# Kernel tuning notes

Hardware: AMD Instinct MI355X
Metric: run time of the kernel (lower is better)

## Reference

```python
import jax, jax.numpy as jnp
import numpy as np


def setup_inputs() -> dict:
    key = jax.random.key(0)
    k1, k2, k3, k4 = jax.random.split(key, 4)
    B, L, H, E = 2, 10000, 8, 64
    NE = 160000
    return {
        "queries": jax.random.normal(k1, (B, L, H, E), dtype=jnp.float32),
        "keys": jax.random.normal(k2, (B, L, H, E), dtype=jnp.float32),
        "values": jax.random.normal(k3, (B, L, H, E), dtype=jnp.float32),
        "adj": jax.random.randint(k4, (2, NE), 0, L, dtype=jnp.int64),
    }


def reference(queries, keys, values, adj):
    # queries/keys/values: [B, L, H, E]; adj: [2, NE] (row 0 = dst group, row 1 = src)
    B, L, H, E = queries.shape
    softmax_temp = 1.0 / (E ** 0.5)
    dst = adj[0]
    src = adj[1]

    # edge-gather dot product: qk[b, e, h] = sum_d q[b, dst[e], h, d] * k[b, src[e], h, d]
    qk = jnp.sum(queries[:, dst] * keys[:, src], axis=-1) * softmax_temp  # [B, NE, H]

    # segment softmax grouped by destination node (dropout is identity at eval)
    qk_e = qk.transpose(1, 0, 2)  # [NE, B, H] (segment ops act on leading axis)
    seg_max = jax.ops.segment_max(qk_e, dst, num_segments=L)  # [L, B, H]
    ex = jnp.exp(qk_e - seg_max[dst])
    seg_sum = jax.ops.segment_sum(ex, dst, num_segments=L)  # [L, B, H]
    alpha = ex / (seg_sum[dst] + 1e-16)  # [NE, B, H]

    # spmm: gather v at src, weight by alpha, scatter-add to dst
    weighted = values[:, src] * alpha.transpose(1, 0, 2)[..., None]  # [B, NE, H, E]
    out = jnp.zeros_like(values).at[:, dst].add(weighted)  # [B, L, H, E]
    return out
```

## Files before the change

### kernel.cpp

```cpp
#include <hip/hip_runtime.h>

#define BB 2
#define HH 8
#define EE 64
#define ROW (HH * EE)
#define HC 4

typedef float vf4 __attribute__((ext_vector_type(4)));

__device__ inline unsigned short f2bf(float f) {
  unsigned int u = __float_as_uint(f);
  u = (u + 0x7fffu + ((u >> 16) & 1u)) >> 16;
  return (unsigned short)u;
}

__global__ __launch_bounds__(256) void convert_hist_kernel(
    const float* __restrict__ k, const float* __restrict__ v,
    unsigned short* __restrict__ kbf, unsigned short* __restrict__ vbf,
    const int* __restrict__ dst, int* __restrict__ counts,
    int n4, int NE) {
  int i = blockIdx.x * blockDim.x + threadIdx.x;
  if (i < n4) {
    vf4 kf = __builtin_nontemporal_load((const vf4*)k + i);
    vf4 vf = __builtin_nontemporal_load((const vf4*)v + i);
    ((ushort4*)kbf)[i] = make_ushort4(f2bf(kf.x), f2bf(kf.y), f2bf(kf.z), f2bf(kf.w));
    ((ushort4*)vbf)[i] = make_ushort4(f2bf(vf.x), f2bf(vf.y), f2bf(vf.z), f2bf(vf.w));
  }
  if (i < NE) {
    atomicAdd(&counts[dst[i]], 1);
  }
}

__global__ __launch_bounds__(1024) void scan_kernel(
    const int* __restrict__ counts_in, int* __restrict__ counts_mut,
    int* __restrict__ offsets, int L) {
  __shared__ int sums[1024];
  int tid = threadIdx.x;
  int chunk = (L + 1023) / 1024;
  int beg = tid * chunk;
  int end = min(beg + chunk, L);
  int s = 0;
  for (int i = beg; i < end; ++i) s += counts_in[i];
  sums[tid] = s;
  __syncthreads();
  for (int off = 1; off < 1024; off <<= 1) {
    int val = 0;
    if (tid >= off) val = sums[tid - off];
    __syncthreads();
    if (tid >= off) sums[tid] += val;
    __syncthreads();
  }
  int run = (tid > 0) ? sums[tid - 1] : 0;
  for (int i = beg; i < end; ++i) {
    offsets[i] = run;
    run += counts_in[i];
    counts_mut[i] = 0;
  }
  if (tid == 1023) offsets[L] = run;
}

__global__ __launch_bounds__(256) void fill_csr_kernel(
    const int* __restrict__ dst, const int* __restrict__ src,
    const int* __restrict__ offsets, int* __restrict__ cursor,
    int* __restrict__ csr_src, int NE) {
  int e = blockIdx.x * blockDim.x + threadIdx.x;
  if (e >= NE) return;
  int d = dst[e];
  int pos = atomicAdd(&cursor[d], 1);
  csr_src[offsets[d] + pos] = src[e];
}

__device__ inline void bf8_unpack(uint4 u, float* f) {
  f[0] = __uint_as_float(u.x << 16);
  f[1] = __uint_as_float(u.x & 0xffff0000u);
  f[2] = __uint_as_float(u.y << 16);
  f[3] = __uint_as_float(u.y & 0xffff0000u);
  f[4] = __uint_as_float(u.z << 16);
  f[5] = __uint_as_float(u.z & 0xffff0000u);
  f[6] = __uint_as_float(u.w << 16);
  f[7] = __uint_as_float(u.w & 0xffff0000u);
}

#define LOAD_HC(KK, VV, TT)                                           \
  _Pragma("unroll") for (int i_ = 0; i_ < HC; ++i_) {                 \
    int e_ = min((TT) + i_, NEm1);                                    \
    unsigned s_ = (unsigned)csr_src[e_];                              \
    KK[i_] = kb_base[s_ * (unsigned)(ROW / 8) + lane];                \
    VV[i_] = vb_base[s_ * (unsigned)(ROW / 8) + lane];                \
  }

#define COMPUTE_HC(KK, VV, TT)                                        \
  do {                                                                \
    float qk_[HC];                                                    \
    float cmax_ = -INFINITY;                                          \
    _Pragma("unroll") for (int i_ = 0; i_ < HC; ++i_) {               \
      float kf_[8];                                                   \
      bf8_unpack(KK[i_], kf_);                                        \
      float p_ = q0.x * kf_[0] + q0.y * kf_[1] + q0.z * kf_[2] +      \
                 q0.w * kf_[3] + q1.x * kf_[4] + q1.y * kf_[5] +      \
                 q1.z * kf_[6] + q1.w * kf_[7];                       \
      p_ += __shfl_xor(p_, 1);                                        \
      p_ += __shfl_xor(p_, 2);                                        \
      p_ += __shfl_xor(p_, 4);                                        \
      p_ = ((TT) + i_ < end) ? p_ : -INFINITY;                        \
      qk_[i_] = p_;                                                   \
      cmax_ = fmaxf(cmax_, p_);                                       \
    }                                                                 \
    if (__any(cmax_ > m)) {        \
      float mnew_ = fmaxf(m, cmax_);                                  \
      float scale_ = __expf(m - mnew_); \
      l_run *= scale_;                                                \
      _Pragma("unroll") for (int j_ = 0; j_ < 8; ++j_) acc[j_] *= scale_; \
      m = mnew_;                                                      \
    }                                                                 \
    _Pragma("unroll") for (int i_ = 0; i_ < HC; ++i_) {               \
      float a_ = __expf(qk_[i_] - m);        \
      l_run += a_;                                                    \
      float vfv_[8];                                                  \
      bf8_unpack(VV[i_], vfv_);                                       \
      _Pragma("unroll") for (int j_ = 0; j_ < 8; ++j_)                \
          acc[j_] += a_ * vfv_[j_];                                   \
    }                                                                 \
  } while (0)

__global__ __launch_bounds__(256, 4) void fused_attn_kernel(
    const float* __restrict__ q, const unsigned short* __restrict__ kbf,
    const unsigned short* __restrict__ vbf, const int* __restrict__ offsets,
    const int* __restrict__ csr_src, float* __restrict__ out, int L, int NE) {
  int wid = blockIdx.x * (blockDim.x >> 6) + (threadIdx.x >> 6);
  int lane = threadIdx.x & 63;
  if (wid >= L * BB) return;
  int d = wid >> 1;
  int b = wid & 1;
  int beg = offsets[d];
  int end = offsets[d + 1];
  const int NEm1 = NE - 1;

  const vf4* qrow = (const vf4*)(q + ((size_t)b * L + d) * ROW);
  vf4 q0 = __builtin_nontemporal_load(qrow + lane * 2 + 0);
  vf4 q1 = __builtin_nontemporal_load(qrow + lane * 2 + 1);
  q0 *= 0.125f;
  q1 *= 0.125f;

  float m = -INFINITY;
  float l_run = 0.0f;
  float acc[8];
#pragma unroll
  for (int i = 0; i < 8; ++i) acc[i] = 0.0f;

  const uint4* kb_base = (const uint4*)(kbf + (size_t)b * L * ROW);
  const uint4* vb_base = (const uint4*)(vbf + (size_t)b * L * ROW);

  uint4 kA[HC], vA[HC], kB[HC], vB[HC];
  int tA = beg;
  int tB = beg + HC;
  if (tA < end) {
    LOAD_HC(kA, vA, tA);
    LOAD_HC(kB, vB, tB);
    for (;;) {
      COMPUTE_HC(kA, vA, tA);
      tA = tB + HC;
      if (tA < end) LOAD_HC(kA, vA, tA);
      if (tB >= end) break;
      COMPUTE_HC(kB, vB, tB);
      tB = tA + HC;
      if (tB < end) LOAD_HC(kB, vB, tB);
      if (tA >= end) break;
    }
  }

  float r = 1.0f / (l_run + 1e-16f);
  vf4* orow = (vf4*)(out + ((size_t)b * L + d) * ROW);
  vf4 o0 = {acc[0] * r, acc[1] * r, acc[2] * r, acc[3] * r};
  vf4 o1 = {acc[4] * r, acc[5] * r, acc[6] * r, acc[7] * r};
  __builtin_nontemporal_store(o0, orow + lane * 2 + 0);
  __builtin_nontemporal_store(o1, orow + lane * 2 + 1);
}

extern "C" void kernel_launch(void* const* d_in, const int* in_sizes, int n_in,
                              void* d_out, int out_size, void* d_ws, size_t ws_size,
                              hipStream_t stream) {
  const float* q = (const float*)d_in[0];
  const float* k = (const float*)d_in[1];
  const float* v = (const float*)d_in[2];
  const int* adj = (const int*)d_in[3];

  const int NE = in_sizes[3] / 2;
  const int L = in_sizes[0] / (BB * HH * EE);
  const int* dst = adj;
  const int* src = adj + NE;
  const int nelem = BB * L * HH * EE;

  char* ws = (char*)d_ws;
  size_t off = 0;
  unsigned short* kbf = (unsigned short*)(ws + off); off += (size_t)nelem * 2;
  unsigned short* vbf = (unsigned short*)(ws + off); off += (size_t)nelem * 2;
  int* counts = (int*)(ws + off);   off += (size_t)L * 4;
  int* offsets = (int*)(ws + off);  off += (size_t)(L + 1) * 4;
  int* csr_src = (int*)(ws + off);  off += (size_t)NE * 4;

  hipMemsetAsync(counts, 0, (size_t)L * 4, stream);

  int n4 = nelem / 4;
  convert_hist_kernel<<<(n4 + 255) / 256, 256, 0, stream>>>(
      k, v, kbf, vbf, dst, counts, n4, NE);

  scan_kernel<<<1, 1024, 0, stream>>>(counts, counts, offsets, L);

  fill_csr_kernel<<<(NE + 255) / 256, 256, 0, stream>>>(
      dst, src, offsets, counts, csr_src, NE);

  int nwaves = L * BB;
  fused_attn_kernel<<<(nwaves + 3) / 4, 256, 0, stream>>>(
      q, kbf, vbf, offsets, csr_src, (float*)d_out, L, NE);
}
```

Baseline: 306.9 us.

## Use grid-stride persistent waves and batched 8-edge loads in fused attention

```diff
diff --git a/kernel.cpp b/kernel.cpp
--- a/kernel.cpp
+++ b/kernel.cpp
@@ -81,100 +81,92 @@
   f[7] = __uint_as_float(u.w & 0xffff0000u);
 }
 
-#define LOAD_HC(KK, VV, TT)                                           \
-  _Pragma("unroll") for (int i_ = 0; i_ < HC; ++i_) {                 \
-    int e_ = min((TT) + i_, NEm1);                                    \
-    unsigned s_ = (unsigned)csr_src[e_];                              \
-    KK[i_] = kb_base[s_ * (unsigned)(ROW / 8) + lane];                \
-    VV[i_] = vb_base[s_ * (unsigned)(ROW / 8) + lane];                \
-  }
-
-#define COMPUTE_HC(KK, VV, TT)                                        \
-  do {                                                                \
-    float qk_[HC];                                                    \
-    float cmax_ = -INFINITY;                                          \
-    _Pragma("unroll") for (int i_ = 0; i_ < HC; ++i_) {               \
-      float kf_[8];                                                   \
-      bf8_unpack(KK[i_], kf_);                                        \
-      float p_ = q0.x * kf_[0] + q0.y * kf_[1] + q0.z * kf_[2] +      \
-                 q0.w * kf_[3] + q1.x * kf_[4] + q1.y * kf_[5] +      \
-                 q1.z * kf_[6] + q1.w * kf_[7];                       \
-      p_ += __shfl_xor(p_, 1);                                        \
-      p_ += __shfl_xor(p_, 2);                                        \
-      p_ += __shfl_xor(p_, 4);                                        \
-      p_ = ((TT) + i_ < end) ? p_ : -INFINITY;                        \
-      qk_[i_] = p_;                                                   \
-      cmax_ = fmaxf(cmax_, p_);                                       \
-    }                                                                 \
-    if (__any(cmax_ > m)) {        \
-      float mnew_ = fmaxf(m, cmax_);                                  \
-      float scale_ = __expf(m - mnew_); \
-      l_run *= scale_;                                                \
-      _Pragma("unroll") for (int j_ = 0; j_ < 8; ++j_) acc[j_] *= scale_; \
-      m = mnew_;                                                      \
-    }                                                                 \
-    _Pragma("unroll") for (int i_ = 0; i_ < HC; ++i_) {               \
-      float a_ = __expf(qk_[i_] - m);        \
-      l_run += a_;                                                    \
-      float vfv_[8];                                                  \
-      bf8_unpack(VV[i_], vfv_);                                       \
-      _Pragma("unroll") for (int j_ = 0; j_ < 8; ++j_)                \
-          acc[j_] += a_ * vfv_[j_];                                   \
-    }                                                                 \
-  } while (0)
-
-__global__ __launch_bounds__(256, 4) void fused_attn_kernel(
+__global__ __launch_bounds__(256) void fused_attn_kernel(
     const float* __restrict__ q, const unsigned short* __restrict__ kbf,
     const unsigned short* __restrict__ vbf, const int* __restrict__ offsets,
-    const int* __restrict__ csr_src, float* __restrict__ out, int L, int NE) {
-  int wid = blockIdx.x * (blockDim.x >> 6) + (threadIdx.x >> 6);
-  int lane = threadIdx.x & 63;
-  if (wid >= L * BB) return;
-  int d = wid >> 1;
-  int b = wid & 1;
-  int beg = offsets[d];
-  int end = offsets[d + 1];
-  const int NEm1 = NE - 1;
-
-  const vf4* qrow = (const vf4*)(q + ((size_t)b * L + d) * ROW);
-  vf4 q0 = __builtin_nontemporal_load(qrow + lane * 2 + 0);
-  vf4 q1 = __builtin_nontemporal_load(qrow + lane * 2 + 1);
-  q0 *= 0.125f;
-  q1 *= 0.125f;
-
-  float m = -INFINITY;
-  float l_run = 0.0f;
-  float acc[8];
-#pragma unroll
-  for (int i = 0; i < 8; ++i) acc[i] = 0.0f;
-
-  const uint4* kb_base = (const uint4*)(kbf + (size_t)b * L * ROW);
-  const uint4* vb_base = (const uint4*)(vbf + (size_t)b * L * ROW);
-
-  uint4 kA[HC], vA[HC], kB[HC], vB[HC];
-  int tA = beg;
-  int tB = beg + HC;
-  if (tA < end) {
-    LOAD_HC(kA, vA, tA);
-    LOAD_HC(kB, vB, tB);
-    for (;;) {
-      COMPUTE_HC(kA, vA, tA);
-      tA = tB + HC;
-      if (tA < end) LOAD_HC(kA, vA, tA);
-      if (tB >= end) break;
-      COMPUTE_HC(kB, vB, tB);
-      tB = tA + HC;
-      if (tB < end) LOAD_HC(kB, vB, tB);
-      if (tA >= end) break;
+    const int* __restrict__ csr_src, float* __restrict__ out, int L) {
+  const int lane = threadIdx.x & 63;
+  const int wslot = blockIdx.x * (blockDim.x >> 6) + (threadIdx.x >> 6);
+  const int wstride = gridDim.x * (blockDim.x >> 6);
+  const int nwid = L * BB;
+
+  for (int wid = wslot; wid < nwid; wid += wstride) {
+    int d = wid >> 1;
+    int b = wid & 1;
+    int beg = offsets[d];
+    int end = offsets[d + 1];
+
+    const vf4* qrow = (const vf4*)(q + ((size_t)b * L + d) * ROW);
+    vf4 q0 = __builtin_nontemporal_load(qrow + lane * 2 + 0);
+    vf4 q1 = __builtin_nontemporal_load(qrow + lane * 2 + 1);
+    q0 *= 0.125f;
+    q1 *= 0.125f;
+
+    float m = -INFINITY;
+    float l_run = 0.0f;
+    float acc[8];
+#pragma unroll
+    for (int i = 0; i < 8; ++i) acc[i] = 0.0f;
+
+    const uint4* kb_base = (const uint4*)(kbf + (size_t)b * L * ROW);
+    const uint4* vb_base = (const uint4*)(vbf + (size_t)b * L * ROW);
+
+    for (int t0 = beg; t0 < end; t0 += 2 * HC) {
+      int cnt = min(2 * HC, end - t0);
+      uint4 kk[2 * HC], vv[2 * HC];
+#pragma unroll
+      for (int i = 0; i < 2 * HC; ++i) {
+        if (i < cnt) {
+          unsigned s = (unsigned)csr_src[t0 + i];
+          kk[i] = kb_base[s * (unsigned)(ROW / 8) + lane];
+          vv[i] = vb_base[s * (unsigned)(ROW / 8) + lane];
+        }
+      }
+      float qk[2 * HC];
+      float cmax = -INFINITY;
+#pragma unroll
+      for (int i = 0; i < 2 * HC; ++i) {
+        qk[i] = -INFINITY;
+        if (i < cnt) {
+          float kf[8];
+          bf8_unpack(kk[i], kf);
+          float p = q0.x * kf[0] + q0.y * kf[1] + q0.z * kf[2] + q0.w * kf[3] +
+                    q1.x * kf[4] + q1.y * kf[5] + q1.z * kf[6] + q1.w * kf[7];
+          p += __shfl_xor(p, 1);
+          p += __shfl_xor(p, 2);
+          p += __shfl_xor(p, 4);
+          qk[i] = p;
+          cmax = fmaxf(cmax, p);
+        }
+      }
+      if (__any(cmax > m)) {
+        float mnew = fmaxf(m, cmax);
+        float scale = __expf(m - mnew);
+        l_run *= scale;
+#pragma unroll
+        for (int i = 0; i < 8; ++i) acc[i] *= scale;
+        m = mnew;
+      }
+#pragma unroll
+      for (int i = 0; i < 2 * HC; ++i) {
+        if (i < cnt) {
+          float a = __expf(qk[i] - m);
+          l_run += a;
+          float vf[8];
+          bf8_unpack(vv[i], vf);
+#pragma unroll
+          for (int j = 0; j < 8; ++j) acc[j] += a * vf[j];
+        }
+      }
     }
-  }
-
-  float r = 1.0f / (l_run + 1e-16f);
-  vf4* orow = (vf4*)(out + ((size_t)b * L + d) * ROW);
-  vf4 o0 = {acc[0] * r, acc[1] * r, acc[2] * r, acc[3] * r};
-  vf4 o1 = {acc[4] * r, acc[5] * r, acc[6] * r, acc[7] * r};
-  __builtin_nontemporal_store(o0, orow + lane * 2 + 0);
-  __builtin_nontemporal_store(o1, orow + lane * 2 + 1);
+
+    float r = 1.0f / (l_run + 1e-16f);
+    vf4* orow = (vf4*)(out + ((size_t)b * L + d) * ROW);
+    vf4 o0 = {acc[0] * r, acc[1] * r, acc[2] * r, acc[3] * r};
+    vf4 o1 = {acc[4] * r, acc[5] * r, acc[6] * r, acc[7] * r};
+    __builtin_nontemporal_store(o0, orow + lane * 2 + 0);
+    __builtin_nontemporal_store(o1, orow + lane * 2 + 1);
+  }
 }
 
 extern "C" void kernel_launch(void* const* d_in, const int* in_sizes, int n_in,
@@ -211,6 +203,7 @@
       dst, src, offsets, counts, csr_src, NE);
 
   int nwaves = L * BB;
-  fused_attn_kernel<<<(nwaves + 3) / 4, 256, 0, stream>>>(
-      q, kbf, vbf, offsets, csr_src, (float*)d_out, L, NE);
-}
+  int nblocks = min(2048, (nwaves + 3) / 4);
+  fused_attn_kernel<<<nblocks, 256, 0, stream>>>(
+      q, kbf, vbf, offsets, csr_src, (float*)d_out, L);
+}
```

Result: faster. 292.1 us (-4.8%).
